# Optimization experiments

Measured on AMD Instinct MI355X. Metric: run time of the kernel, lower is better.

Reference implementation:

```python
import jax, jax.numpy as jnp
import numpy as np

BATCH, LENGTH, FEAT, RANK = 4096, 128, 4, 64
SCALE = 1.0 / np.sqrt(RANK)  # keep 128-step matrix chain numerically stable


def setup_inputs() -> dict:
    key = jax.random.key(0)
    k1, k2, k3, k4 = jax.random.split(key, 4)
    return {
        "input_data": jax.random.normal(k1, (BATCH, LENGTH, FEAT), dtype=jnp.float32),
        "first_core": jax.random.normal(k2, (FEAT, RANK), dtype=jnp.float32) * SCALE,
        "mid_cores": jax.random.normal(k3, (LENGTH - 2, RANK, FEAT, RANK), dtype=jnp.float32) * SCALE,
        "last_core": jax.random.normal(k4, (RANK, FEAT), dtype=jnp.float32) * SCALE,
    }


def reference(input_data, first_core, mid_cores, last_core):
    # input_data: [b, L, f] -> site-major [L, b, f]
    x = jnp.transpose(input_data, (1, 0, 2))
    # Per-site contraction with the physical (feature) index.
    v0 = jnp.einsum("ir,bi->br", first_core, x[0])            # [b, r]
    mid_mats = jnp.einsum("slir,sbi->sblr", mid_cores, x[1:-1])  # [S, b, r, r]
    last_vec = jnp.einsum("li,bi->bl", last_core, x[-1])      # [b, r]

    # Sequential tensor-train chain: v <- v @ M_s for each middle site.
    def step(v, mat):
        return jnp.einsum("bl,blr->br", v, mat), None

    v, _ = jax.lax.scan(step, v0, mid_mats)
    # Final contraction against last site vector -> [b, 1]
    out = jnp.sum(v * last_vec, axis=-1, keepdims=True)
    return out
```

## Files before the change

kernel.cpp:

```cpp
#include <hip/hip_runtime.h>
#include <stdint.h>

#define NSITES 126
#define XPITCH 516
#define VPH    72

typedef _Float16 half8_t  __attribute__((ext_vector_type(8)));
typedef float    float4_t __attribute__((ext_vector_type(4)));

#define LBAR() asm volatile("s_waitcnt lgkmcnt(0)\n\ts_barrier" ::: "memory")
#define WAITV(N) asm volatile("s_waitcnt vmcnt(" #N ")" ::: "memory")
#define TIE8(F) asm volatile("" : "+v"(F[0]), "+v"(F[1]), "+v"(F[2]), "+v"(F[3]), \
                                  "+v"(F[4]), "+v"(F[5]), "+v"(F[6]), "+v"(F[7]))

__device__ __forceinline__ void aload(half8_t& d, const void* p) {
    asm volatile("global_load_dwordx4 %0, %1, off" : "=v"(d) : "v"(p));
}

__global__ __launch_bounds__(256) void repack_g(const float* __restrict__ mid,
                                                _Float16* __restrict__ gt) {
    const int F = blockIdx.x * 256 + threadIdx.x;
    const int lane = F & 63, w = (F >> 6) & 3, h = (F >> 8) & 1, i = (F >> 9) & 3;
    const int s = F >> 11;
    const int q = lane >> 4, c = lane & 15;
    const float* src = mid + (size_t)s * 16384 + (32 * h + 8 * q) * 256 + i * 64 + w * 16 + c;
    half8_t o;
#pragma unroll
    for (int j = 0; j < 8; ++j) o[j] = (_Float16)src[j * 256];
    ((half8_t*)gt)[F] = o;
}

__global__ __launch_bounds__(512, 2) void tt_chain(
    const float* __restrict__ x,
    const float* __restrict__ first,
    const float* __restrict__ last,
    const _Float16* __restrict__ gt,
    float* __restrict__ out) {

    __shared__ __align__(16) _Float16 vbuf[2][16 * VPH];
    __shared__ float xbuf[16 * XPITCH];
    __shared__ int   eacc[16];

    const int tid  = threadIdx.x;
    const int w    = tid >> 6;
    const int team = w >> 2;
    const int wv   = w & 3;
    const int lane = tid & 63;
    const int q    = lane >> 4;
    const int c    = lane & 15;
    const int b0   = blockIdx.x * 16;

    {
        const int bb = tid >> 5, seg = tid & 31;
        const float4_t* src = (const float4_t*)(x + (size_t)(b0 + bb) * 512);
        float4_t* dst = (float4_t*)(xbuf + bb * XPITCH);
#pragma unroll
        for (int k = 0; k < 4; ++k) dst[seg + 32 * k] = src[seg + 32 * k];
    }
    if (tid < 16) eacc[tid] = 0;
    __syncthreads();

    if (tid < 256) {
        const int bb = tid >> 4, rq = tid & 15;
        const float xs0 = xbuf[bb * XPITCH + 0], xs1 = xbuf[bb * XPITCH + 1];
        const float xs2 = xbuf[bb * XPITCH + 2], xs3 = xbuf[bb * XPITCH + 3];
#pragma unroll
        for (int k = 0; k < 4; ++k) {
            const int r = rq * 4 + k;
            vbuf[0][bb * VPH + r] = (_Float16)(
                xs0 * first[r] + xs1 * first[64 + r] + xs2 * first[128 + r] + xs3 * first[192 + r]);
        }
    }

    half8_t F0[8], F1[8], F2[8];
    const char* gbase = (const char*)gt + wv * 1024 + lane * 16;
    auto LOAD = [&](int s, half8_t* F) {
        const char* p = gbase + (size_t)s * 32768;
#pragma unroll
        for (int ih = 0; ih < 8; ++ih) aload(F[ih], p + ih * 4096);
    };

    float4_t xs[4];
    auto XRD = [&](int s) {
#pragma unroll
        for (int jj = 0; jj < 4; ++jj)
            xs[jj] = *(const float4_t*)(xbuf + (q * 4 + jj) * XPITCH + (s + 1) * 4);
    };

    if (team == 0) { LOAD(0, F0); LOAD(2, F1); LOAD(4, F2); XRD(0); }
    else           { LOAD(1, F0); LOAD(3, F1); }
    LBAR();

    auto STEP = [&](int s, half8_t* F) {
        const int p = s & 1;
        const _Float16* vr = &vbuf[p][c * VPH];
        half8_t af0 = *(const half8_t*)(vr + q * 8);
        half8_t af1 = *(const half8_t*)(vr + 32 + q * 8);

        WAITV(16);
        TIE8(F);

        if ((s & 7) == 0 && s != 0) {
            float a[16];
#pragma unroll
            for (int k = 0; k < 8; ++k) { a[k] = (float)af0[k]; a[8 + k] = (float)af1[k]; }
            float m = 0.f;
#pragma unroll
            for (int k = 0; k < 16; ++k) m = fmaxf(m, fabsf(a[k]));
            m = fmaxf(m, __shfl_xor(m, 16));
            m = fmaxf(m, __shfl_xor(m, 32));
            int e = 0;
            if (m > 0.f) frexpf(m, &e);
            const float sc = ldexpf(1.0f, -e);
#pragma unroll
            for (int k = 0; k < 8; ++k) {
                af0[k] = (_Float16)(a[k] * sc);
                af1[k] = (_Float16)(a[8 + k] * sc);
            }
            if (tid < 16) eacc[tid] += e;
        }

        float4_t acc[4];
#pragma unroll
        for (int i = 0; i < 4; ++i) {
            float4_t z = {0.f, 0.f, 0.f, 0.f};
            z = __builtin_amdgcn_mfma_f32_16x16x32_f16(af0, F[i * 2 + 0], z, 0, 0, 0);
            z = __builtin_amdgcn_mfma_f32_16x16x32_f16(af1, F[i * 2 + 1], z, 0, 0, 0);
            acc[i] = z;
        }

#pragma unroll
        for (int jj = 0; jj < 4; ++jj) {
            const float vn = xs[jj].x * acc[0][jj] + xs[jj].y * acc[1][jj] +
                             xs[jj].z * acc[2][jj] + xs[jj].w * acc[3][jj];
            vbuf[p ^ 1][(q * 4 + jj) * VPH + wv * 16 + c] = (_Float16)vn;
        }
    };

    for (int B = 0; B < NSITES; B += 6) {
        if (team == 0) STEP(B + 0, F0);
        else { LOAD((B + 5 < NSITES) ? B + 5 : 125, F2); XRD(B + 1); }
        LBAR();
        if (team == 1) STEP(B + 1, F0);
        else { LOAD((B + 6 < NSITES) ? B + 6 : 124, F0); XRD(B + 2); }
        LBAR();
        if (team == 0) STEP(B + 2, F1);
        else { LOAD((B + 7 < NSITES) ? B + 7 : 125, F0); XRD(B + 3); }
        LBAR();
        if (team == 1) STEP(B + 3, F1);
        else { LOAD((B + 8 < NSITES) ? B + 8 : 124, F1); XRD(B + 4); }
        LBAR();
        if (team == 0) STEP(B + 4, F2);
        else { LOAD((B + 9 < NSITES) ? B + 9 : 125, F1); XRD(B + 5); }
        LBAR();
        if (team == 1) STEP(B + 5, F2);
        else { LOAD((B + 10 < NSITES) ? B + 10 : 124, F2); XRD(B + 6); }
        LBAR();
    }
    WAITV(0);

    if (tid < 256) {
        const int bb = tid >> 4, rq = tid & 15;
        const float x0 = xbuf[bb * XPITCH + 508], x1 = xbuf[bb * XPITCH + 509];
        const float x2 = xbuf[bb * XPITCH + 510], x3 = xbuf[bb * XPITCH + 511];
        float dot = 0.f;
#pragma unroll
        for (int k = 0; k < 4; ++k) {
            const int r = rq * 4 + k;
            const float lv = last[r * 4 + 0] * x0 + last[r * 4 + 1] * x1 +
                             last[r * 4 + 2] * x2 + last[r * 4 + 3] * x3;
            dot += lv * (float)vbuf[0][bb * VPH + r];
        }
#pragma unroll
        for (int o = 8; o > 0; o >>= 1) dot += __shfl_xor(dot, o, 16);
        if (rq == 0) out[b0 + bb] = ldexpf(dot, eacc[bb]);
    }
}

extern "C" void kernel_launch(void* const* d_in, const int* in_sizes, int n_in,
                              void* d_out, int out_size, void* d_ws, size_t ws_size,
                              hipStream_t stream) {
    (void)in_sizes; (void)n_in; (void)out_size; (void)ws_size;
    const float* x     = (const float*)d_in[0];
    const float* first = (const float*)d_in[1];
    const float* mid   = (const float*)d_in[2];
    const float* last  = (const float*)d_in[3];
    float* out = (float*)d_out;
    _Float16* gt = (_Float16*)d_ws;

    repack_g<<<1008, 256, 0, stream>>>(mid, gt);
    tt_chain<<<256, 512, 0, stream>>>(x, first, last, gt, out);
}
```

Before: 111.0 us.

## Process 32 batch rows per block to reuse loaded core fragments across two MFMA groups

Each block now handles two 16-row batch groups, so every set of core fragments loaded from global memory feeds twice as many MFMAs. The grid is halved to 128 blocks, which cuts redundant global traffic for the repacked cores. The costs are double the LDS use for xbuf and vbuf, more registers per step, and fewer blocks than the GPU's CU count, which lowers parallelism on a latency-bound sequential chain.

```diff
diff --git a/kernel.cpp b/kernel.cpp
--- a/kernel.cpp
+++ b/kernel.cpp
@@ -37,9 +37,9 @@
     const _Float16* __restrict__ gt,
     float* __restrict__ out) {
 
-    __shared__ __align__(16) _Float16 vbuf[2][16 * VPH];
-    __shared__ float xbuf[16 * XPITCH];
-    __shared__ int   eacc[16];
+    __shared__ __align__(16) _Float16 vbuf[2][2][16 * VPH];
+    __shared__ float xbuf[32 * XPITCH];
+    __shared__ int   eacc[32];
 
     const int tid  = threadIdx.x;
     const int w    = tid >> 6;
@@ -48,27 +48,31 @@
     const int lane = tid & 63;
     const int q    = lane >> 4;
     const int c    = lane & 15;
-    const int b0   = blockIdx.x * 16;
+    const int b0   = blockIdx.x * 32;
 
     {
-        const int bb = tid >> 5, seg = tid & 31;
+        const int bb = tid >> 4, seg = tid & 15;
         const float4_t* src = (const float4_t*)(x + (size_t)(b0 + bb) * 512);
         float4_t* dst = (float4_t*)(xbuf + bb * XPITCH);
 #pragma unroll
-        for (int k = 0; k < 4; ++k) dst[seg + 32 * k] = src[seg + 32 * k];
-    }
-    if (tid < 16) eacc[tid] = 0;
+        for (int k = 0; k < 8; ++k) dst[seg + 16 * k] = src[seg + 16 * k];
+    }
+    if (tid < 32) eacc[tid] = 0;
     __syncthreads();
 
     if (tid < 256) {
         const int bb = tid >> 4, rq = tid & 15;
-        const float xs0 = xbuf[bb * XPITCH + 0], xs1 = xbuf[bb * XPITCH + 1];
-        const float xs2 = xbuf[bb * XPITCH + 2], xs3 = xbuf[bb * XPITCH + 3];
-#pragma unroll
-        for (int k = 0; k < 4; ++k) {
-            const int r = rq * 4 + k;
-            vbuf[0][bb * VPH + r] = (_Float16)(
-                xs0 * first[r] + xs1 * first[64 + r] + xs2 * first[128 + r] + xs3 * first[192 + r]);
+#pragma unroll
+        for (int g = 0; g < 2; ++g) {
+            const int row = g * 16 + bb;
+            const float xs0 = xbuf[row * XPITCH + 0], xs1 = xbuf[row * XPITCH + 1];
+            const float xs2 = xbuf[row * XPITCH + 2], xs3 = xbuf[row * XPITCH + 3];
+#pragma unroll
+            for (int k = 0; k < 4; ++k) {
+                const int r = rq * 4 + k;
+                vbuf[g][0][bb * VPH + r] = (_Float16)(
+                    xs0 * first[r] + xs1 * first[64 + r] + xs2 * first[128 + r] + xs3 * first[192 + r]);
+            }
         }
     }
 
@@ -80,60 +84,78 @@
         for (int ih = 0; ih < 8; ++ih) aload(F[ih], p + ih * 4096);
     };
 
-    float4_t xs[4];
+    float4_t xsA[4], xsB[4];
     auto XRD = [&](int s) {
 #pragma unroll
-        for (int jj = 0; jj < 4; ++jj)
-            xs[jj] = *(const float4_t*)(xbuf + (q * 4 + jj) * XPITCH + (s + 1) * 4);
+        for (int jj = 0; jj < 4; ++jj) {
+            xsA[jj] = *(const float4_t*)(xbuf + (q * 4 + jj) * XPITCH + (s + 1) * 4);
+            xsB[jj] = *(const float4_t*)(xbuf + (16 + q * 4 + jj) * XPITCH + (s + 1) * 4);
+        }
     };
 
     if (team == 0) { LOAD(0, F0); LOAD(2, F1); LOAD(4, F2); XRD(0); }
     else           { LOAD(1, F0); LOAD(3, F1); }
     LBAR();
 
+    auto RN = [&](half8_t& af0, half8_t& af1) -> int {
+        float a[16];
+#pragma unroll
+        for (int k = 0; k < 8; ++k) { a[k] = (float)af0[k]; a[8 + k] = (float)af1[k]; }
+        float m = 0.f;
+#pragma unroll
+        for (int k = 0; k < 16; ++k) m = fmaxf(m, fabsf(a[k]));
+        m = fmaxf(m, __shfl_xor(m, 16));
+        m = fmaxf(m, __shfl_xor(m, 32));
+        int e = 0;
+        if (m > 0.f) frexpf(m, &e);
+        const float sc = ldexpf(1.0f, -e);
+#pragma unroll
+        for (int k = 0; k < 8; ++k) {
+            af0[k] = (_Float16)(a[k] * sc);
+            af1[k] = (_Float16)(a[8 + k] * sc);
+        }
+        return e;
+    };
+
     auto STEP = [&](int s, half8_t* F) {
         const int p = s & 1;
-        const _Float16* vr = &vbuf[p][c * VPH];
-        half8_t af0 = *(const half8_t*)(vr + q * 8);
-        half8_t af1 = *(const half8_t*)(vr + 32 + q * 8);
+        const _Float16* vrA = &vbuf[0][p][c * VPH];
+        const _Float16* vrB = &vbuf[1][p][c * VPH];
+        half8_t afA0 = *(const half8_t*)(vrA + q * 8);
+        half8_t afA1 = *(const half8_t*)(vrA + 32 + q * 8);
+        half8_t afB0 = *(const half8_t*)(vrB + q * 8);
+        half8_t afB1 = *(const half8_t*)(vrB + 32 + q * 8);
 
         WAITV(16);
         TIE8(F);
 
         if ((s & 7) == 0 && s != 0) {
-            float a[16];
-#pragma unroll
-            for (int k = 0; k < 8; ++k) { a[k] = (float)af0[k]; a[8 + k] = (float)af1[k]; }
-            float m = 0.f;
-#pragma unroll
-            for (int k = 0; k < 16; ++k) m = fmaxf(m, fabsf(a[k]));
-            m = fmaxf(m, __shfl_xor(m, 16));
-            m = fmaxf(m, __shfl_xor(m, 32));
-            int e = 0;
-            if (m > 0.f) frexpf(m, &e);
-            const float sc = ldexpf(1.0f, -e);
-#pragma unroll
-            for (int k = 0; k < 8; ++k) {
-                af0[k] = (_Float16)(a[k] * sc);
-                af1[k] = (_Float16)(a[8 + k] * sc);
-            }
-            if (tid < 16) eacc[tid] += e;
-        }
-
-        float4_t acc[4];
+            const int eA = RN(afA0, afA1);
+            const int eB = RN(afB0, afB1);
+            if (tid < 16) { eacc[tid] += eA; eacc[16 + tid] += eB; }
+        }
+
+        float4_t accA[4], accB[4];
 #pragma unroll
         for (int i = 0; i < 4; ++i) {
-            float4_t z = {0.f, 0.f, 0.f, 0.f};
-            z = __builtin_amdgcn_mfma_f32_16x16x32_f16(af0, F[i * 2 + 0], z, 0, 0, 0);
-            z = __builtin_amdgcn_mfma_f32_16x16x32_f16(af1, F[i * 2 + 1], z, 0, 0, 0);
-            acc[i] = z;
+            float4_t zA = {0.f, 0.f, 0.f, 0.f};
+            zA = __builtin_amdgcn_mfma_f32_16x16x32_f16(afA0, F[i * 2 + 0], zA, 0, 0, 0);
+            zA = __builtin_amdgcn_mfma_f32_16x16x32_f16(afA1, F[i * 2 + 1], zA, 0, 0, 0);
+            accA[i] = zA;
+            float4_t zB = {0.f, 0.f, 0.f, 0.f};
+            zB = __builtin_amdgcn_mfma_f32_16x16x32_f16(afB0, F[i * 2 + 0], zB, 0, 0, 0);
+            zB = __builtin_amdgcn_mfma_f32_16x16x32_f16(afB1, F[i * 2 + 1], zB, 0, 0, 0);
+            accB[i] = zB;
         }
 
 #pragma unroll
         for (int jj = 0; jj < 4; ++jj) {
-            const float vn = xs[jj].x * acc[0][jj] + xs[jj].y * acc[1][jj] +
-                             xs[jj].z * acc[2][jj] + xs[jj].w * acc[3][jj];
-            vbuf[p ^ 1][(q * 4 + jj) * VPH + wv * 16 + c] = (_Float16)vn;
+            const float vnA = xsA[jj].x * accA[0][jj] + xsA[jj].y * accA[1][jj] +
+                              xsA[jj].z * accA[2][jj] + xsA[jj].w * accA[3][jj];
+            vbuf[0][p ^ 1][(q * 4 + jj) * VPH + wv * 16 + c] = (_Float16)vnA;
+            const float vnB = xsB[jj].x * accB[0][jj] + xsB[jj].y * accB[1][jj] +
+                              xsB[jj].z * accB[2][jj] + xsB[jj].w * accB[3][jj];
+            vbuf[1][p ^ 1][(q * 4 + jj) * VPH + wv * 16 + c] = (_Float16)vnB;
         }
     };
 
@@ -161,19 +183,23 @@
 
     if (tid < 256) {
         const int bb = tid >> 4, rq = tid & 15;
-        const float x0 = xbuf[bb * XPITCH + 508], x1 = xbuf[bb * XPITCH + 509];
-        const float x2 = xbuf[bb * XPITCH + 510], x3 = xbuf[bb * XPITCH + 511];
-        float dot = 0.f;
-#pragma unroll
-        for (int k = 0; k < 4; ++k) {
-            const int r = rq * 4 + k;
-            const float lv = last[r * 4 + 0] * x0 + last[r * 4 + 1] * x1 +
-                             last[r * 4 + 2] * x2 + last[r * 4 + 3] * x3;
-            dot += lv * (float)vbuf[0][bb * VPH + r];
-        }
-#pragma unroll
-        for (int o = 8; o > 0; o >>= 1) dot += __shfl_xor(dot, o, 16);
-        if (rq == 0) out[b0 + bb] = ldexpf(dot, eacc[bb]);
+#pragma unroll
+        for (int g = 0; g < 2; ++g) {
+            const int row = g * 16 + bb;
+            const float x0 = xbuf[row * XPITCH + 508], x1 = xbuf[row * XPITCH + 509];
+            const float x2 = xbuf[row * XPITCH + 510], x3 = xbuf[row * XPITCH + 511];
+            float dot = 0.f;
+#pragma unroll
+            for (int k = 0; k < 4; ++k) {
+                const int r = rq * 4 + k;
+                const float lv = last[r * 4 + 0] * x0 + last[r * 4 + 1] * x1 +
+                                 last[r * 4 + 2] * x2 + last[r * 4 + 3] * x3;
+                dot += lv * (float)vbuf[g][0][bb * VPH + r];
+            }
+#pragma unroll
+            for (int o = 8; o > 0; o >>= 1) dot += __shfl_xor(dot, o, 16);
+            if (rq == 0) out[b0 + row] = ldexpf(dot, eacc[g * 16 + bb]);
+        }
     }
 }
 
@@ -189,5 +215,5 @@
     _Float16* gt = (_Float16*)d_ws;
 
     repack_g<<<1008, 256, 0, stream>>>(mid, gt);
-    tt_chain<<<256, 512, 0, stream>>>(x, first, last, gt, out);
-}
+    tt_chain<<<128, 512, 0, stream>>>(x, first, last, gt, out);
+}
```

New measurement: 124.2 us. 11.8% more time.
